# Kernel tuning notes

Measured on AMD Instinct MI355X. Metric: run time of the kernel, lower is better.

## Reference

```python
import jax, jax.numpy as jnp
import numpy as np

B, S, D, E = 2, 2048, 1024, 16  # batch, cutoff (seq), dmodel, n_experts


def setup_inputs() -> dict:
    key = jax.random.key(0)
    k = jax.random.split(key, 6)
    scale = 1.0 / np.sqrt(D)
    return {
        "x": jax.random.normal(k[0], (B, S, D), dtype=jnp.float32),
        "gate": jax.random.normal(k[1], (D, E), dtype=jnp.float32) * scale,
        "W1": jax.random.normal(k[2], (E, D, D), dtype=jnp.float32) * scale,  # lin1: Linear(dmodel, dmodel*E), split per expert
        "b1": jnp.zeros((E, D), dtype=jnp.float32),
        "W2": jax.random.normal(k[3], (E, D, D), dtype=jnp.float32) * scale,  # lin2: Linear(dmodel*E, dmodel), split per expert
        "b2": jnp.zeros((D,), dtype=jnp.float32),
        "topk": 256,
    }


def reference(x, gate, W1, b1, W2, b2, topk):
    # Expert-choice gating: softmax over the token (cutoff) axis per expert.
    logits = jnp.einsum("bsd,de->bse", x, gate)            # (B, S, E)
    probs = jax.nn.softmax(logits, axis=1)                  # softmax over tokens
    # Each expert selects its top-k tokens.
    g, idx = jax.lax.top_k(jnp.swapaxes(probs, 1, 2), topk)  # (B, E, k)
    # Gather selected tokens: (B, E, k, D)
    xin = jnp.take_along_axis(x[:, None, :, :], idx[..., None], axis=2)
    # Per-expert 2-layer FFN (hidden size = dmodel, per width = dmodel*n_experts)
    h = jax.nn.relu(jnp.einsum("bekd,edf->bekf", xin, W1) + b1[None, :, None, :])
    out = jnp.einsum("bekf,efd->bekd", h, W2) + b2           # (B, E, k, D)
    weighted = out * g[..., None]
    # Scatter-add back to token positions.
    y = jnp.zeros_like(x)
    b_idx = jnp.arange(x.shape[0])[:, None, None]            # (B, 1, 1)
    y = y.at[b_idx, idx].add(weighted)
    return y
```

## Files before the change

### kernel.cpp

```cpp
#include <hip/hip_runtime.h>
#include <stdint.h>
#include <math.h>

constexpr int CB = 2;
constexpr int CS = 2048;
constexpr int CD = 1024;
constexpr int CE = 16;
constexpr int CK = 256;

typedef short bf16x8 __attribute__((ext_vector_type(8)));
typedef float f32x4 __attribute__((ext_vector_type(4)));

typedef __attribute__((address_space(1))) const unsigned int gu32;
typedef __attribute__((address_space(3))) unsigned int lu32;
typedef __attribute__((address_space(3))) unsigned short lds_us;

__device__ __forceinline__ void async16(const void* g, lds_us* l) {
    __builtin_amdgcn_global_load_lds((gu32*)g, (lu32*)l, 16, 0, 0);
}

__device__ __forceinline__ bf16x8 ds_read128(const lds_us* p) {
    bf16x8 v;
    asm volatile("ds_read_b128 %0, %1" : "=v"(v) : "v"(p));
    return v;
}

__device__ inline unsigned short f2bf(float f) {
    union { float f; uint32_t u; } v; v.f = f;
    uint32_t u = v.u;
    uint32_t r = (u + 0x7FFFu + ((u >> 16) & 1u)) >> 16;
    return (unsigned short)r;
}

__global__ __launch_bounds__(256)
void logits_part_kernel(const float* __restrict__ x,
                        const float* __restrict__ gate,
                        float* __restrict__ part) {
    const int tt = blockIdx.x;
    const int dt = blockIdx.y;
    const int tid = threadIdx.x;

    __shared__ float Xs[256 * 17];

    float acc[CE];
#pragma unroll
    for (int e = 0; e < CE; e++) acc[e] = 0.0f;

    const int tokl = tid >> 2;
    const int c4 = (tid & 3) << 2;

    for (int dch = 0; dch < 4; dch++) {
        const int dbase = dt * 64 + dch * 16;
        __syncthreads();
#pragma unroll
        for (int q = 0; q < 4; q++) {
            const int tok = q * 64 + tokl;
            const f32x4 v = *(const f32x4*)(x + ((size_t)(tt * 256 + tok)) * CD + dbase + c4);
            Xs[tok * 17 + c4 + 0] = v[0];
            Xs[tok * 17 + c4 + 1] = v[1];
            Xs[tok * 17 + c4 + 2] = v[2];
            Xs[tok * 17 + c4 + 3] = v[3];
        }
        __syncthreads();
#pragma unroll
        for (int d = 0; d < 16; d++) {
            const float xv = Xs[tid * 17 + d];
            const float* gr = gate + (size_t)(dbase + d) * CE;
#pragma unroll
            for (int e = 0; e < CE; e++) acc[e] = fmaf(xv, gr[e], acc[e]);
        }
    }
    float* pr = part + ((size_t)dt * (CB * CS) + tt * 256 + tid) * CE;
#pragma unroll
    for (int e = 0; e < CE; e++) pr[e] = acc[e];
}

__global__ __launch_bounds__(256)
void logits_reduce_kernel(const float* __restrict__ part,
                          float* __restrict__ logits) {
    const int i = blockIdx.x * 256 + threadIdx.x;
    float s = 0.0f;
#pragma unroll
    for (int p = 0; p < 16; p++) s += part[(size_t)p * (CB * CS * CE) + i];
    logits[i] = s;
}

__global__ void topk_kernel(const float* __restrict__ logits,
                            int* __restrict__ idx_out,
                            float* __restrict__ g_out) {
    const int be = blockIdx.x;
    const int b = be >> 4, e = be & 15;
    const int tid = threadIdx.x;
    const int lane = tid & 63, wid = tid >> 6;

    __shared__ float redf[4];
    __shared__ int hist[256];
    __shared__ int wsum[4];
    __shared__ int sh_bin, sh_rank;
    __shared__ int scnt, eqc;
    __shared__ int eqbuf[CS];

    float lv[8], p[8];
    unsigned int uv[8];
#pragma unroll
    for (int j = 0; j < 8; j++) {
        const int s = tid + j * 256;
        lv[j] = logits[((size_t)(b * CS + s)) * CE + e];
    }
    float m = lv[0];
#pragma unroll
    for (int j = 1; j < 8; j++) m = fmaxf(m, lv[j]);
#pragma unroll
    for (int o = 32; o > 0; o >>= 1) m = fmaxf(m, __shfl_down(m, o));
    if (lane == 0) redf[wid] = m;
    __syncthreads();
    m = fmaxf(fmaxf(redf[0], redf[1]), fmaxf(redf[2], redf[3]));
    __syncthreads();
    float lsum = 0.0f;
#pragma unroll
    for (int j = 0; j < 8; j++) {
        p[j] = expf(lv[j] - m);
        uv[j] = __float_as_uint(p[j]);
        lsum += p[j];
    }
#pragma unroll
    for (int o = 32; o > 0; o >>= 1) lsum += __shfl_down(lsum, o);
    if (lane == 0) redf[wid] = lsum;
    __syncthreads();
    const float total = redf[0] + redf[1] + redf[2] + redf[3];
    const float inv_total = 1.0f / total;

    unsigned int prefix = 0;
    int kneed = CK;
    for (int pass = 0; pass < 4; pass++) {
        const int shift = 24 - 8 * pass;
        __syncthreads();
        hist[tid] = 0;
        __syncthreads();
        const unsigned int hmask = (pass == 0) ? 0u : (0xFFFFFFFFu << (shift + 8));
#pragma unroll
        for (int j = 0; j < 8; j++)
            if ((uv[j] & hmask) == prefix)
                atomicAdd(&hist[(uv[j] >> shift) & 255], 1);
        __syncthreads();
        const int own = hist[tid];
        int s = own;
#pragma unroll
        for (int o = 1; o < 64; o <<= 1) {
            int t = __shfl_down(s, o);
            if (lane + o < 64) s += t;
        }
        if (lane == 0) wsum[wid] = s;
        __syncthreads();
        int above = 0;
        for (int ww = wid + 1; ww < 4; ww++) above += wsum[ww];
        const int incl = s + above;
        if (incl >= kneed && (incl - own) < kneed) {
            sh_bin = tid;
            sh_rank = kneed - (incl - own);
        }
        __syncthreads();
        prefix |= ((unsigned int)sh_bin) << shift;
        kneed = sh_rank;
    }
    const unsigned int v = prefix;
    const int quota = kneed;

    if (tid == 0) { scnt = 0; eqc = 0; }
    __syncthreads();
#pragma unroll
    for (int j = 0; j < 8; j++) {
        const int s = tid + j * 256;
        if (uv[j] > v) {
            const int pos = atomicAdd(&scnt, 1);
            idx_out[be * CK + pos] = s;
            g_out[be * CK + pos] = p[j] * inv_total;
        } else if (uv[j] == v) {
            const int pos = atomicAdd(&eqc, 1);
            eqbuf[pos] = s;
        }
    }
    __syncthreads();
    if (tid == 0) {
        const int cgt = scnt;
        const int n = eqc;
        const float gv = __uint_as_float(v) * inv_total;
        if (n > quota) {
            for (int i = 0; i < quota; i++) {
                int mn = i;
                for (int k2 = i + 1; k2 < n; k2++)
                    if (eqbuf[k2] < eqbuf[mn]) mn = k2;
                const int t2 = eqbuf[i]; eqbuf[i] = eqbuf[mn]; eqbuf[mn] = t2;
            }
        }
        for (int i = 0; i < quota; i++) {
            idx_out[be * CK + cgt + i] = eqbuf[i];
            g_out[be * CK + cgt + i] = gv;
        }
    }
}

__global__ void gather_kernel(const float* __restrict__ x,
                              const int* __restrict__ idx_ws,
                              unsigned short* __restrict__ xinbuf) {
    const int row = blockIdx.x;
    const int be = row >> 8;
    const int b = be >> 4;
    const int tok = idx_ws[row];
    const int c0 = threadIdx.x * 4;
    const f32x4 f = *(const f32x4*)(x + ((size_t)b * CS + tok) * CD + c0);
    union { unsigned short u[4]; uint2 v; } t;
    t.u[0] = f2bf(f[0]); t.u[1] = f2bf(f[1]); t.u[2] = f2bf(f[2]); t.u[3] = f2bf(f[3]);
    *(uint2*)(xinbuf + (size_t)row * CD + c0) = t.v;
}

__global__ __launch_bounds__(256)
void wt_kernel(const float* __restrict__ W, unsigned short* __restrict__ Wt) {
    const int kt = blockIdx.x, nt = blockIdx.y, e = blockIdx.z;
    const float* src = W + (size_t)e * CD * CD;
    unsigned short* dst = Wt + (size_t)e * CD * CD;
    const int tid = threadIdx.x;
    __shared__ unsigned short T[64 * 64];

    const int kr = tid >> 4;
    const int n4 = (tid & 15) << 2;
#pragma unroll
    for (int it = 0; it < 4; it++) {
        const int k = it * 16 + kr;
        const f32x4 v = *(const f32x4*)(src + (size_t)(kt * 64 + k) * CD + nt * 64 + n4);
        const int pp = k >> 4;
        const int klo = k & 15;
#pragma unroll
        for (int i = 0; i < 4; i++) {
            const int n = n4 + i;
            T[n * 64 + ((pp ^ ((n >> 2) & 3)) << 4) + klo] = f2bf(v[i]);
        }
    }
    __syncthreads();
    const int n = tid >> 2;
    const int pp = tid & 3;
    const int sw = pp ^ ((n >> 2) & 3);
    const uint4 a = *(const uint4*)&T[n * 64 + (sw << 4)];
    const uint4 b = *(const uint4*)&T[n * 64 + (sw << 4) + 8];
    unsigned short* drow = dst + (size_t)(nt * 64 + n) * CD + kt * 64 + pp * 16;
    *(uint4*)drow = a;
    *(uint4*)(drow + 8) = b;
}

template <int PHASE>
__global__ __launch_bounds__(256, 2)
void ffn_gemm(const unsigned short* __restrict__ Ain,
              const unsigned short* __restrict__ Wt,
              const float* __restrict__ bias,
              unsigned short* __restrict__ hout,
              const int* __restrict__ idx_ws,
              const float* __restrict__ g_ws,
              float* __restrict__ y) {
    const int id = blockIdx.x;
    const int e = (id & 7) | (((id >> 3) & 1) << 3);
    const int b = (id >> 4) & 1;
    const int mtile = (id >> 5) & 1;
    const int ntile = id >> 6;
    const int be = b * 16 + e;
    const int tid = threadIdx.x;
    const int w = tid >> 6, l = tid & 63;
    const int wm = w & 1, wn = w >> 1;
    const int quad = l >> 4, lr = l & 15;

    __shared__ __align__(16) unsigned short As_s[3][128 * 32];
    __shared__ __align__(16) unsigned short Bs_s[3][128 * 32];

    f32x4 acc[4][4];
    const f32x4 zz = {0.f, 0.f, 0.f, 0.f};
#pragma unroll
    for (int mi = 0; mi < 4; mi++)
#pragma unroll
        for (int ni = 0; ni < 4; ni++) acc[mi][ni] = zz;

    const unsigned short* Abase = Ain + ((size_t)be * CK + mtile * 128) * CD;
    const unsigned short* Bbase = Wt + ((size_t)e * CD + ntile * 128) * CD;

    int c_c[2];
    size_t goff[2];
#pragma unroll
    for (int j = 0; j < 2; j++) {
        const int c = (w + j * 4) * 64 + l;
        c_c[j] = c;
        const int row = c >> 2;
        const int kc = (c & 3) ^ ((row >> 1) & 3);
        goff[j] = (size_t)row * CD + kc * 8;
    }

    const int fpos = (quad ^ ((lr >> 1) & 3)) * 8;

    lds_us* pa0 = (lds_us*)As_s[0]; lds_us* pa1 = (lds_us*)As_s[1]; lds_us* pa2 = (lds_us*)As_s[2];
    lds_us* pb0 = (lds_us*)Bs_s[0]; lds_us* pb1 = (lds_us*)Bs_s[1]; lds_us* pb2 = (lds_us*)Bs_s[2];

#pragma unroll
    for (int j = 0; j < 2; j++) {
        async16(Abase + goff[j], pa0 + c_c[j] * 8);
        async16(Bbase + goff[j], pb0 + c_c[j] * 8);
    }
#pragma unroll
    for (int j = 0; j < 2; j++) {
        async16(Abase + goff[j] + 32, pa1 + c_c[j] * 8);
        async16(Bbase + goff[j] + 32, pb1 + c_c[j] * 8);
    }

    for (int ks = 0; ks < 32; ks++) {
        if (ks < 30) {
            const int k2 = (ks + 2) * 32;
#pragma unroll
            for (int j = 0; j < 2; j++) {
                async16(Abase + goff[j] + k2, pa2 + c_c[j] * 8);
                async16(Bbase + goff[j] + k2, pb2 + c_c[j] * 8);
            }
            asm volatile("s_waitcnt vmcnt(8)" ::: "memory");
        } else if (ks == 30) {
            asm volatile("s_waitcnt vmcnt(4)" ::: "memory");
        } else {
            asm volatile("s_waitcnt vmcnt(0)" ::: "memory");
        }
        asm volatile("s_barrier" ::: "memory");

        bf16x8 af[4], bfr[4];
#pragma unroll
        for (int mi = 0; mi < 4; mi++)
            af[mi] = ds_read128(pa0 + (wm * 64 + mi * 16 + lr) * 32 + fpos);
#pragma unroll
        for (int ni = 0; ni < 4; ni++)
            bfr[ni] = ds_read128(pb0 + (wn * 64 + ni * 16 + lr) * 32 + fpos);
        asm volatile("s_waitcnt lgkmcnt(0)"
                     : "+v"(af[0]), "+v"(af[1]), "+v"(af[2]), "+v"(af[3]),
                       "+v"(bfr[0]), "+v"(bfr[1]), "+v"(bfr[2]), "+v"(bfr[3])
                     :: "memory");
#pragma unroll
        for (int mi = 0; mi < 4; mi++)
#pragma unroll
            for (int ni = 0; ni < 4; ni++)
                acc[mi][ni] = __builtin_amdgcn_mfma_f32_16x16x32_bf16(
                    af[mi], bfr[ni], acc[mi][ni], 0, 0, 0);

        asm volatile("s_barrier" ::: "memory");
        lds_us* t = pa0; pa0 = pa1; pa1 = pa2; pa2 = t;
        t = pb0; pb0 = pb1; pb1 = pb2; pb2 = t;
    }

    const int gn_base = ntile * 128 + wn * 64;
    if (PHASE == 0) {
#pragma unroll
        for (int mi = 0; mi < 4; mi++)
#pragma unroll
            for (int r = 0; r < 4; r++) {
                const int slot = mtile * 128 + wm * 64 + mi * 16 + quad * 4 + r;
                unsigned short* outrow = hout + ((size_t)be * CK + slot) * CD;
#pragma unroll
                for (int ni = 0; ni < 4; ni++) {
                    const int col = gn_base + ni * 16 + lr;
                    float hv = acc[mi][ni][r] + bias[e * CD + col];
                    hv = fmaxf(hv, 0.0f);
                    outrow[col] = f2bf(hv);
                }
            }
    } else {
#pragma unroll
        for (int mi = 0; mi < 4; mi++)
#pragma unroll
            for (int r = 0; r < 4; r++) {
                const int slot = mtile * 128 + wm * 64 + mi * 16 + quad * 4 + r;
                const int tok = idx_ws[be * CK + slot];
                const float gval = g_ws[be * CK + slot];
                float* yrow = y + ((size_t)b * CS + tok) * CD;
#pragma unroll
                for (int ni = 0; ni < 4; ni++) {
                    const int col = gn_base + ni * 16 + lr;
                    const float val = (acc[mi][ni][r] + bias[col]) * gval;
                    atomicAdd(&yrow[col], val);
                }
            }
    }
}

extern "C" void kernel_launch(void* const* d_in, const int* in_sizes, int n_in,
                              void* d_out, int out_size, void* d_ws, size_t ws_size,
                              hipStream_t stream) {
    const float* x    = (const float*)d_in[0];
    const float* gate = (const float*)d_in[1];
    const float* W1   = (const float*)d_in[2];
    const float* b1   = (const float*)d_in[3];
    const float* W2   = (const float*)d_in[4];
    const float* b2   = (const float*)d_in[5];
    float* y = (float*)d_out;

    char* ws = (char*)d_ws;
    float* logits = (float*)ws;
    int* idxw = (int*)(ws + 262144);
    float* gw = (float*)(ws + 294912);
    unsigned short* xinbuf = (unsigned short*)(ws + 327680);
    unsigned short* hbuf = (unsigned short*)(ws + 17104896);
    float* partbuf = (float*)(ws + 17104896);
    unsigned short* wtbuf = (unsigned short*)(ws + 33882112);

    logits_part_kernel<<<dim3(16, 16), 256, 0, stream>>>(x, gate, partbuf);
    logits_reduce_kernel<<<CB * CS * CE / 256, 256, 0, stream>>>(partbuf, logits);
    topk_kernel<<<CB * CE, 256, 0, stream>>>(logits, idxw, gw);
    gather_kernel<<<CB * CE * CK, 256, 0, stream>>>(x, idxw, xinbuf);
    wt_kernel<<<dim3(16, 16, CE), 256, 0, stream>>>(W1, wtbuf);
    hipMemsetAsync(d_out, 0, (size_t)CB * CS * CD * sizeof(float), stream);
    ffn_gemm<0><<<512, 256, 0, stream>>>(xinbuf, wtbuf, b1, hbuf, idxw, gw, y);
    wt_kernel<<<dim3(16, 16, CE), 256, 0, stream>>>(W2, wtbuf);
    ffn_gemm<1><<<512, 256, 0, stream>>>(hbuf, wtbuf, b2, nullptr, idxw, gw, y);
}
```

Before: 283.1 us.

## Fuse prep kernels, zero output in logits kernel, and shrink GEMM tiles

New measurement: 293.4 us. 3.6% more time.

```diff
diff --git a/kernel.cpp b/kernel.cpp
--- a/kernel.cpp
+++ b/kernel.cpp
@@ -35,10 +35,19 @@
 __global__ __launch_bounds__(256)
 void logits_part_kernel(const float* __restrict__ x,
                         const float* __restrict__ gate,
-                        float* __restrict__ part) {
+                        float* __restrict__ part,
+                        float* __restrict__ y) {
     const int tt = blockIdx.x;
     const int dt = blockIdx.y;
     const int tid = threadIdx.x;
+
+    {
+        const int bb = dt * 16 + tt;
+        float* yb = y + (size_t)bb * 16384 + tid * 4;
+        const f32x4 z = {0.f, 0.f, 0.f, 0.f};
+#pragma unroll
+        for (int i = 0; i < 16; i++) *(f32x4*)(yb + i * 1024) = z;
+    }
 
     __shared__ float Xs[256 * 17];
 
@@ -75,17 +84,7 @@
     for (int e = 0; e < CE; e++) pr[e] = acc[e];
 }
 
-__global__ __launch_bounds__(256)
-void logits_reduce_kernel(const float* __restrict__ part,
-                          float* __restrict__ logits) {
-    const int i = blockIdx.x * 256 + threadIdx.x;
-    float s = 0.0f;
-#pragma unroll
-    for (int p = 0; p < 16; p++) s += part[(size_t)p * (CB * CS * CE) + i];
-    logits[i] = s;
-}
-
-__global__ void topk_kernel(const float* __restrict__ logits,
+__global__ void topk_kernel(const float* __restrict__ part,
                             int* __restrict__ idx_out,
                             float* __restrict__ g_out) {
     const int be = blockIdx.x;
@@ -105,7 +104,11 @@
 #pragma unroll
     for (int j = 0; j < 8; j++) {
         const int s = tid + j * 256;
-        lv[j] = logits[((size_t)(b * CS + s)) * CE + e];
+        const size_t base = ((size_t)(b * CS + s)) * CE + e;
+        float sum = 0.0f;
+#pragma unroll
+        for (int pp = 0; pp < 16; pp++) sum += part[(size_t)pp * (CB * CS * CE) + base];
+        lv[j] = sum;
     }
     float m = lv[0];
 #pragma unroll
@@ -200,27 +203,11 @@
     }
 }
 
-__global__ void gather_kernel(const float* __restrict__ x,
-                              const int* __restrict__ idx_ws,
-                              unsigned short* __restrict__ xinbuf) {
-    const int row = blockIdx.x;
-    const int be = row >> 8;
-    const int b = be >> 4;
-    const int tok = idx_ws[row];
-    const int c0 = threadIdx.x * 4;
-    const f32x4 f = *(const f32x4*)(x + ((size_t)b * CS + tok) * CD + c0);
-    union { unsigned short u[4]; uint2 v; } t;
-    t.u[0] = f2bf(f[0]); t.u[1] = f2bf(f[1]); t.u[2] = f2bf(f[2]); t.u[3] = f2bf(f[3]);
-    *(uint2*)(xinbuf + (size_t)row * CD + c0) = t.v;
-}
-
-__global__ __launch_bounds__(256)
-void wt_kernel(const float* __restrict__ W, unsigned short* __restrict__ Wt) {
-    const int kt = blockIdx.x, nt = blockIdx.y, e = blockIdx.z;
+__device__ __forceinline__
+void wt_body(const float* __restrict__ W, unsigned short* __restrict__ Wt,
+             int kt, int nt, int e, int tid, unsigned short* T) {
     const float* src = W + (size_t)e * CD * CD;
     unsigned short* dst = Wt + (size_t)e * CD * CD;
-    const int tid = threadIdx.x;
-    __shared__ unsigned short T[64 * 64];
 
     const int kr = tid >> 4;
     const int n4 = (tid & 15) << 2;
@@ -247,8 +234,37 @@
     *(uint4*)(drow + 8) = b;
 }
 
+__global__ __launch_bounds__(256)
+void wt_kernel(const float* __restrict__ W, unsigned short* __restrict__ Wt) {
+    __shared__ unsigned short T[64 * 64];
+    wt_body(W, Wt, blockIdx.x, blockIdx.y, blockIdx.z, threadIdx.x, T);
+}
+
+__global__ __launch_bounds__(256)
+void prep_kernel(const float* __restrict__ W1, unsigned short* __restrict__ Wt,
+                 const float* __restrict__ x, const int* __restrict__ idx_ws,
+                 unsigned short* __restrict__ xinbuf) {
+    __shared__ unsigned short T[64 * 64];
+    const int bx = blockIdx.x;
+    if (bx < 4096) {
+        wt_body(W1, Wt, bx & 15, (bx >> 4) & 15, bx >> 8, threadIdx.x, T);
+    } else {
+        const int row = bx - 4096;
+        const int be = row >> 8;
+        const int b = be >> 4;
+        const int tok = idx_ws[row];
+        const int c0 = threadIdx.x * 4;
+        const f32x4 f = *(const f32x4*)(x + ((size_t)b * CS + tok) * CD + c0);
+        union { unsigned short u[4]; uint2 v; } t;
+        t.u[0] = f2bf(f[0]); t.u[1] = f2bf(f[1]); t.u[2] = f2bf(f[2]); t.u[3] = f2bf(f[3]);
+        *(uint2*)(xinbuf + (size_t)row * CD + c0) = t.v;
+    }
+}
+
+#define MFMA16(A_, B_, C_) __builtin_amdgcn_mfma_f32_16x16x32_bf16((A_), (B_), (C_), 0, 0, 0)
+
 template <int PHASE>
-__global__ __launch_bounds__(256, 2)
+__global__ __launch_bounds__(256, 4)
 void ffn_gemm(const unsigned short* __restrict__ Ain,
               const unsigned short* __restrict__ Wt,
               const float* __restrict__ bias,
@@ -257,105 +273,111 @@
               const float* __restrict__ g_ws,
               float* __restrict__ y) {
     const int id = blockIdx.x;
-    const int e = (id & 7) | (((id >> 3) & 1) << 3);
-    const int b = (id >> 4) & 1;
-    const int mtile = (id >> 5) & 1;
-    const int ntile = id >> 6;
-    const int be = b * 16 + e;
+    const int xcd = id & 7;
+    const int q = id >> 3;
+    const int e = ((q & 1) << 3) | xcd;
+    const int b = (q >> 1) & 1;
+    const int mtile = (q >> 2) & 3;
+    const int ntile = q >> 4;
+    const int be = b * CE + e;
     const int tid = threadIdx.x;
     const int w = tid >> 6, l = tid & 63;
-    const int wm = w & 1, wn = w >> 1;
     const int quad = l >> 4, lr = l & 15;
 
-    __shared__ __align__(16) unsigned short As_s[3][128 * 32];
+    __shared__ __align__(16) unsigned short As_s[3][64 * 32];
     __shared__ __align__(16) unsigned short Bs_s[3][128 * 32];
 
-    f32x4 acc[4][4];
+    f32x4 acc[4][2];
     const f32x4 zz = {0.f, 0.f, 0.f, 0.f};
 #pragma unroll
     for (int mi = 0; mi < 4; mi++)
 #pragma unroll
-        for (int ni = 0; ni < 4; ni++) acc[mi][ni] = zz;
-
-    const unsigned short* Abase = Ain + ((size_t)be * CK + mtile * 128) * CD;
+        for (int ni = 0; ni < 2; ni++) acc[mi][ni] = zz;
+
+    const unsigned short* Abase = Ain + ((size_t)be * CK + mtile * 64) * CD;
     const unsigned short* Bbase = Wt + ((size_t)e * CD + ntile * 128) * CD;
 
-    int c_c[2];
-    size_t goff[2];
+    const int rA = tid >> 2;
+    const int cA = (tid & 3) ^ (rA & 3);
+    const size_t gA = (size_t)rA * CD + cA * 8;
+    const int dA = tid * 8;
+    size_t gB[2]; int dB[2];
 #pragma unroll
     for (int j = 0; j < 2; j++) {
-        const int c = (w + j * 4) * 64 + l;
-        c_c[j] = c;
-        const int row = c >> 2;
-        const int kc = (c & 3) ^ ((row >> 1) & 3);
-        goff[j] = (size_t)row * CD + kc * 8;
-    }
-
-    const int fpos = (quad ^ ((lr >> 1) & 3)) * 8;
+        const int u = tid + j * 256;
+        const int rB = u >> 2;
+        const int cB = (u & 3) ^ (rB & 3);
+        gB[j] = (size_t)rB * CD + cB * 8;
+        dB[j] = u * 8;
+    }
+
+    const int sc = (quad ^ (lr & 3)) * 8;
+    int offA[4], offB[2];
+#pragma unroll
+    for (int mi = 0; mi < 4; mi++) offA[mi] = (mi * 16 + lr) * 32 + sc;
+#pragma unroll
+    for (int ni = 0; ni < 2; ni++) offB[ni] = (w * 32 + ni * 16 + lr) * 32 + sc;
 
     lds_us* pa0 = (lds_us*)As_s[0]; lds_us* pa1 = (lds_us*)As_s[1]; lds_us* pa2 = (lds_us*)As_s[2];
     lds_us* pb0 = (lds_us*)Bs_s[0]; lds_us* pb1 = (lds_us*)Bs_s[1]; lds_us* pb2 = (lds_us*)Bs_s[2];
 
-#pragma unroll
-    for (int j = 0; j < 2; j++) {
-        async16(Abase + goff[j], pa0 + c_c[j] * 8);
-        async16(Bbase + goff[j], pb0 + c_c[j] * 8);
-    }
-#pragma unroll
-    for (int j = 0; j < 2; j++) {
-        async16(Abase + goff[j] + 32, pa1 + c_c[j] * 8);
-        async16(Bbase + goff[j] + 32, pb1 + c_c[j] * 8);
-    }
-
-    for (int ks = 0; ks < 32; ks++) {
-        if (ks < 30) {
-            const int k2 = (ks + 2) * 32;
-#pragma unroll
-            for (int j = 0; j < 2; j++) {
-                async16(Abase + goff[j] + k2, pa2 + c_c[j] * 8);
-                async16(Bbase + goff[j] + k2, pb2 + c_c[j] * 8);
-            }
-            asm volatile("s_waitcnt vmcnt(8)" ::: "memory");
-        } else if (ks == 30) {
-            asm volatile("s_waitcnt vmcnt(4)" ::: "memory");
+    async16(Abase + gA, pa0 + dA);
+    async16(Bbase + gB[0], pb0 + dB[0]);
+    async16(Bbase + gB[1], pb0 + dB[1]);
+    async16(Abase + gA + 32, pa1 + dA);
+    async16(Bbase + gB[0] + 32, pb1 + dB[0]);
+    async16(Bbase + gB[1] + 32, pb1 + dB[1]);
+
+    for (int t = 0; t < 32; t++) {
+        if (t < 30) {
+            const int k2 = (t + 2) * 32;
+            async16(Abase + gA + k2, pa2 + dA);
+            async16(Bbase + gB[0] + k2, pb2 + dB[0]);
+            async16(Bbase + gB[1] + k2, pb2 + dB[1]);
+            asm volatile("s_waitcnt vmcnt(6)" ::: "memory");
+        } else if (t == 30) {
+            asm volatile("s_waitcnt vmcnt(3)" ::: "memory");
         } else {
             asm volatile("s_waitcnt vmcnt(0)" ::: "memory");
         }
         asm volatile("s_barrier" ::: "memory");
 
-        bf16x8 af[4], bfr[4];
+        bf16x8 a0, a1, a2, a3, b0, b1;
+        a0 = ds_read128(pa0 + offA[0]);
+        a1 = ds_read128(pa0 + offA[1]);
+        a2 = ds_read128(pa0 + offA[2]);
+        a3 = ds_read128(pa0 + offA[3]);
+        b0 = ds_read128(pb0 + offB[0]);
+        b1 = ds_read128(pb0 + offB[1]);
+        asm volatile("s_waitcnt lgkmcnt(0)"
+                     : "+v"(a0), "+v"(a1), "+v"(a2), "+v"(a3), "+v"(b0), "+v"(b1)
+                     :: "memory");
+        __builtin_amdgcn_s_setprio(1);
+        acc[0][0] = MFMA16(a0, b0, acc[0][0]);
+        acc[1][0] = MFMA16(a1, b0, acc[1][0]);
+        acc[2][0] = MFMA16(a2, b0, acc[2][0]);
+        acc[3][0] = MFMA16(a3, b0, acc[3][0]);
+        acc[0][1] = MFMA16(a0, b1, acc[0][1]);
+        acc[1][1] = MFMA16(a1, b1, acc[1][1]);
+        acc[2][1] = MFMA16(a2, b1, acc[2][1]);
+        acc[3][1] = MFMA16(a3, b1, acc[3][1]);
+        __builtin_amdgcn_s_setprio(0);
+        asm volatile("s_barrier" ::: "memory");
+
+        lds_us* tp = pa0; pa0 = pa1; pa1 = pa2; pa2 = tp;
+        tp = pb0; pb0 = pb1; pb1 = pb2; pb2 = tp;
+    }
+
+    const int gn_base = ntile * 128 + w * 32;
+    if (PHASE == 0) {
 #pragma unroll
         for (int mi = 0; mi < 4; mi++)
-            af[mi] = ds_read128(pa0 + (wm * 64 + mi * 16 + lr) * 32 + fpos);
-#pragma unroll
-        for (int ni = 0; ni < 4; ni++)
-            bfr[ni] = ds_read128(pb0 + (wn * 64 + ni * 16 + lr) * 32 + fpos);
-        asm volatile("s_waitcnt lgkmcnt(0)"
-                     : "+v"(af[0]), "+v"(af[1]), "+v"(af[2]), "+v"(af[3]),
-                       "+v"(bfr[0]), "+v"(bfr[1]), "+v"(bfr[2]), "+v"(bfr[3])
-                     :: "memory");
-#pragma unroll
-        for (int mi = 0; mi < 4; mi++)
-#pragma unroll
-            for (int ni = 0; ni < 4; ni++)
-                acc[mi][ni] = __builtin_amdgcn_mfma_f32_16x16x32_bf16(
-                    af[mi], bfr[ni], acc[mi][ni], 0, 0, 0);
-
-        asm volatile("s_barrier" ::: "memory");
-        lds_us* t = pa0; pa0 = pa1; pa1 = pa2; pa2 = t;
-        t = pb0; pb0 = pb1; pb1 = pb2; pb2 = t;
-    }
-
-    const int gn_base = ntile * 128 + wn * 64;
-    if (PHASE == 0) {
-#pragma unroll
-        for (int mi = 0; mi < 4; mi++)
 #pragma unroll
             for (int r = 0; r < 4; r++) {
-                const int slot = mtile * 128 + wm * 64 + mi * 16 + quad * 4 + r;
+                const int slot = mtile * 64 + mi * 16 + quad * 4 + r;
                 unsigned short* outrow = hout + ((size_t)be * CK + slot) * CD;
 #pragma unroll
-                for (int ni = 0; ni < 4; ni++) {
+                for (int ni = 0; ni < 2; ni++) {
                     const int col = gn_base + ni * 16 + lr;
                     float hv = acc[mi][ni][r] + bias[e * CD + col];
                     hv = fmaxf(hv, 0.0f);
@@ -367,12 +389,12 @@
         for (int mi = 0; mi < 4; mi++)
 #pragma unroll
             for (int r = 0; r < 4; r++) {
-                const int slot = mtile * 128 + wm * 64 + mi * 16 + quad * 4 + r;
+                const int slot = mtile * 64 + mi * 16 + quad * 4 + r;
                 const int tok = idx_ws[be * CK + slot];
                 const float gval = g_ws[be * CK + slot];
                 float* yrow = y + ((size_t)b * CS + tok) * CD;
 #pragma unroll
-                for (int ni = 0; ni < 4; ni++) {
+                for (int ni = 0; ni < 2; ni++) {
                     const int col = gn_base + ni * 16 + lr;
                     const float val = (acc[mi][ni][r] + bias[col]) * gval;
                     atomicAdd(&yrow[col], val);
@@ -393,7 +415,6 @@
     float* y = (float*)d_out;
 
     char* ws = (char*)d_ws;
-    float* logits = (float*)ws;
     int* idxw = (int*)(ws + 262144);
     float* gw = (float*)(ws + 294912);
     unsigned short* xinbuf = (unsigned short*)(ws + 327680);
@@ -401,13 +422,10 @@
     float* partbuf = (float*)(ws + 17104896);
     unsigned short* wtbuf = (unsigned short*)(ws + 33882112);
 
-    logits_part_kernel<<<dim3(16, 16), 256, 0, stream>>>(x, gate, partbuf);
-    logits_reduce_kernel<<<CB * CS * CE / 256, 256, 0, stream>>>(partbuf, logits);
-    topk_kernel<<<CB * CE, 256, 0, stream>>>(logits, idxw, gw);
-    gather_kernel<<<CB * CE * CK, 256, 0, stream>>>(x, idxw, xinbuf);
-    wt_kernel<<<dim3(16, 16, CE), 256, 0, stream>>>(W1, wtbuf);
-    hipMemsetAsync(d_out, 0, (size_t)CB * CS * CD * sizeof(float), stream);
-    ffn_gemm<0><<<512, 256, 0, stream>>>(xinbuf, wtbuf, b1, hbuf, idxw, gw, y);
+    logits_part_kernel<<<dim3(16, 16), 256, 0, stream>>>(x, gate, partbuf, y);
+    topk_kernel<<<CB * CE, 256, 0, stream>>>(partbuf, idxw, gw);
+    prep_kernel<<<4096 + CB * CE * CK, 256, 0, stream>>>(W1, wtbuf, x, idxw, xinbuf);
+    ffn_gemm<0><<<1024, 256, 0, stream>>>(xinbuf, wtbuf, b1, hbuf, idxw, gw, y);
     wt_kernel<<<dim3(16, 16, CE), 256, 0, stream>>>(W2, wtbuf);
-    ffn_gemm<1><<<512, 256, 0, stream>>>(hbuf, wtbuf, b2, nullptr, idxw, gw, y);
-}
+    ffn_gemm<1><<<1024, 256, 0, stream>>>(hbuf, wtbuf, b2, nullptr, idxw, gw, y);
+}
```
